# Kernel tuning notes

Hardware: AMD Instinct MI355X
Metric: run time of the kernel (lower is better)

## Reference

```python
import jax, jax.numpy as jnp
import numpy as np

EMBED_DIM = 1024
NUM_HEADS = 16
HEAD_DIM = EMBED_DIM // NUM_HEADS
SEG_LEN = 1024  # all segment_lengths equal, dilation_rate == 1


def setup_inputs() -> dict:
    key = jax.random.key(0)
    k1, k2, k3 = jax.random.split(key, 3)
    B, S, E = 2, 4096, EMBED_DIM
    x = jax.random.normal(k1, (B, S, E), dtype=jnp.float32)
    w_qkv = jax.random.normal(k2, (3 * E, E), dtype=jnp.float32) * (E ** -0.5)
    b_qkv = jnp.zeros((3 * E,), dtype=jnp.float32)
    w_out = jax.random.normal(k3, (E, E), dtype=jnp.float32) * (E ** -0.5)
    b_out = jnp.zeros((E,), dtype=jnp.float32)
    return {"x": x, "w_qkv": w_qkv, "b_qkv": b_qkv, "w_out": w_out, "b_out": b_out}


def reference(x, w_qkv, b_qkv, w_out, b_out):
    B, S, E = x.shape
    H, Dh = NUM_HEADS, HEAD_DIM
    scale = 1.0 / np.sqrt(Dh).astype(np.float32)
    # QKV projection
    qkv = x @ w_qkv.T + b_qkv                      # [B, S, 3E]
    qkv = qkv.reshape(B, S, 3, H, Dh).transpose(2, 0, 3, 1, 4)  # [3, B, H, S, Dh]
    q, k, v = qkv[0], qkv[1], qkv[2]
    # Segments tile the sequence; each query attends only within its segment
    # (block-diagonal attention; online-softmax combine across segments is
    # trivial since the segments are disjoint in the query dimension).
    n = S // SEG_LEN
    q = q.reshape(B, H, n, SEG_LEN, Dh)
    k = k.reshape(B, H, n, SEG_LEN, Dh)
    v = v.reshape(B, H, n, SEG_LEN, Dh)
    scores = jnp.einsum("bhnqd,bhnkd->bhnqk", q, k) * scale
    attn = jax.nn.softmax(scores, axis=-1)
    out = jnp.einsum("bhnqk,bhnkd->bhnqd", attn, v)  # [B, H, n, seg, Dh]
    out = out.reshape(B, H, S, Dh).transpose(0, 2, 1, 3).reshape(B, S, E)
    return out @ w_out.T + b_out
```

## Files before the change

kernel.cpp:

```cpp
#include <hip/hip_runtime.h>

typedef __bf16 bf16x8 __attribute__((ext_vector_type(8)));
typedef float f32x4 __attribute__((ext_vector_type(4)));

#define SL2E 0.18033688011112042f

__device__ __forceinline__ unsigned short f2bf(float f) {
  union { float f; unsigned u; } v; v.f = f;
  unsigned r = v.u + 0x7fffu + ((v.u >> 16) & 1u);
  return (unsigned short)(r >> 16);
}

__device__ __forceinline__ float fast_exp2(float x) {
#if __has_builtin(__builtin_amdgcn_exp2f)
  return __builtin_amdgcn_exp2f(x);
#else
  return exp2f(x);
#endif
}

__device__ __forceinline__ unsigned pack_bf2(float lo, float hi) {
  union { float f; unsigned u; } a, b;
  a.f = lo; b.f = hi;
#if __has_builtin(__builtin_amdgcn_perm)
  return __builtin_amdgcn_perm(b.u + 0x7fffu, a.u + 0x7fffu, 0x07060302u);
#else
  return ((b.u + 0x7fffu) & 0xffff0000u) | ((a.u + 0x7fffu) >> 16);
#endif
}

__device__ __forceinline__ void gload16(const unsigned short* g, unsigned short* l) {
  __builtin_amdgcn_global_load_lds(
      (const __attribute__((address_space(1))) unsigned int*)g,
      (__attribute__((address_space(3))) unsigned int*)l, 16, 0, 0);
}

__global__ __launch_bounds__(256) void f32_to_bf16_all(
    const float* __restrict__ x, const float* __restrict__ wq, const float* __restrict__ wo,
    unsigned short* __restrict__ xb, unsigned short* __restrict__ wqb, unsigned short* __restrict__ wob) {
  int i = blockIdx.x * 256 + threadIdx.x;
  const float* src; unsigned short* dst; int off;
  if (i < 2097152) { src = x; dst = xb; off = i; }
  else if (i < 2883584) { src = wq; dst = wqb; off = i - 2097152; }
  else if (i < 3145728) { src = wo; dst = wob; off = i - 2883584; }
  else return;
  float4 v = ((const float4*)src)[off];
  ushort4 o;
  o.x = f2bf(v.x); o.y = f2bf(v.y); o.z = f2bf(v.z); o.w = f2bf(v.w);
  ((ushort4*)dst)[off] = o;
}


__global__ __launch_bounds__(256) void gemm_qkv(
    const unsigned short* __restrict__ A,
    const unsigned short* __restrict__ Bt,
    const float* __restrict__ bias,
    unsigned short* __restrict__ Qb,
    unsigned short* __restrict__ Kb,
    unsigned short* __restrict__ Vtb) {
  const int K = 1024;
  __shared__ unsigned short As[128 * 64];
  __shared__ unsigned short Bs[128 * 64];
  int tid = threadIdx.x;
  int m0 = blockIdx.x * 128, n0 = blockIdx.y * 128;
  int w = tid >> 6, lane = tid & 63, l15 = lane & 15, quad = lane >> 4;
  int wm = (w & 1) * 64, wn = (w >> 1) * 64;

  f32x4 acc[4][4] = {};

  int rs = w * 32 + (lane >> 3);
  int cs = ((lane & 7) ^ (lane >> 3)) * 8;
  const unsigned short* Ag = A + (m0 + rs) * K + cs;
  const unsigned short* Bg = Bt + (n0 + rs) * K + cs;
  unsigned short* Asl = As + w * 2048;
  unsigned short* Bsl = Bs + w * 2048;

  int t = n0 >> 10;
  int b = m0 >> 12;

  if (t != 2) {
    for (int kt = 0; kt < K; kt += 64) {
      __syncthreads();
#pragma unroll
      for (int i = 0; i < 4; ++i) {
        gload16(Ag + i * 8 * K + kt, Asl + i * 512);
        gload16(Bg + i * 8 * K + kt, Bsl + i * 512);
      }
      __syncthreads();
#pragma unroll
      for (int kk = 0; kk < 2; ++kk) {
        int swk = (((kk * 4 + quad) ^ (l15 & 7))) * 8;
        bf16x8 af[4], bfr[4];
#pragma unroll
        for (int i = 0; i < 4; ++i) af[i] = *(const bf16x8*)(As + (wm + i * 16 + l15) * 64 + swk);
#pragma unroll
        for (int j = 0; j < 4; ++j) bfr[j] = *(const bf16x8*)(Bs + (wn + j * 16 + l15) * 64 + swk);
#pragma unroll
        for (int j = 0; j < 4; ++j)
#pragma unroll
          for (int i = 0; i < 4; ++i)
            acc[j][i] = __builtin_amdgcn_mfma_f32_16x16x32_bf16(bfr[j], af[i], acc[j][i], 0, 0, 0);
      }
    }
    unsigned short* dst = (t == 0) ? Qb : Kb;
    float sc = (t == 0) ? SL2E : 1.0f;
    int h = ((n0 + wn) >> 6) & 15;
    int head_base = (b * 16 + h) * 4096 * 64;
    int s_base = (m0 & 4095) + wm;
#pragma unroll
    for (int j = 0; j < 4; ++j) {
      int d0 = j * 16 + quad * 4;
      float4 bv = *(const float4*)(bias + n0 + wn + d0);
#pragma unroll
      for (int i = 0; i < 4; ++i) {
        int s = s_base + i * 16 + l15;
        ushort4 pk;
        pk.x = f2bf((acc[j][i][0] + bv.x) * sc);
        pk.y = f2bf((acc[j][i][1] + bv.y) * sc);
        pk.z = f2bf((acc[j][i][2] + bv.z) * sc);
        pk.w = f2bf((acc[j][i][3] + bv.w) * sc);
        *(ushort4*)(dst + head_base + s * 64 + d0) = pk;
      }
    }
  } else {
    for (int kt = 0; kt < K; kt += 64) {
      __syncthreads();
#pragma unroll
      for (int i = 0; i < 4; ++i) {
        gload16(Ag + i * 8 * K + kt, Asl + i * 512);
        gload16(Bg + i * 8 * K + kt, Bsl + i * 512);
      }
      __syncthreads();
#pragma unroll
      for (int kk = 0; kk < 2; ++kk) {
        int swk = (((kk * 4 + quad) ^ (l15 & 7))) * 8;
        bf16x8 af[4], bfr[4];
#pragma unroll
        for (int i = 0; i < 4; ++i) af[i] = *(const bf16x8*)(As + (wm + i * 16 + l15) * 64 + swk);
#pragma unroll
        for (int j = 0; j < 4; ++j) bfr[j] = *(const bf16x8*)(Bs + (wn + j * 16 + l15) * 64 + swk);
#pragma unroll
        for (int i = 0; i < 4; ++i)
#pragma unroll
          for (int j = 0; j < 4; ++j)
            acc[i][j] = __builtin_amdgcn_mfma_f32_16x16x32_bf16(af[i], bfr[j], acc[i][j], 0, 0, 0);
      }
    }
    int sblk = (m0 & 4095) + wm + quad * 4;
#pragma unroll
    for (int j = 0; j < 4; ++j) {
      int n_j = n0 + wn + j * 16 + l15;
      float bv = bias[n_j];
      int h = (n_j >> 6) & 15, d = n_j & 63;
      int vbase = ((b * 16 + h) * 64 + d) * 4096;
#pragma unroll
      for (int i = 0; i < 4; ++i) {
        int s = sblk + i * 16;
        ushort4 pk;
        pk.x = f2bf(acc[i][j][0] + bv);
        pk.y = f2bf(acc[i][j][1] + bv);
        pk.z = f2bf(acc[i][j][2] + bv);
        pk.w = f2bf(acc[i][j][3] + bv);
        *(ushort4*)(Vtb + vbase + s) = pk;
      }
    }
  }
}

#define LDP 72
#define SWZ(r, cg) ((((r) * 8) + ((cg) ^ ((r) & 7))) * 8)

__global__ __launch_bounds__(256) void attn_k(
    const unsigned short* __restrict__ Qb,
    const unsigned short* __restrict__ Kb,
    const unsigned short* __restrict__ Vtb,
    unsigned short* __restrict__ Ab) {
  __shared__ unsigned short KV[2][2][4096];
  __shared__ unsigned short Ps[2][4][16 * LDP];

  int tid = threadIdx.x;
  int idx = blockIdx.x;
  int grp = idx & 127, qblk = idx >> 7;
  int seg = grp & 3, h = (grp >> 2) & 15, b = grp >> 6;
  int w = tid >> 6, lane = tid & 63, l15 = lane & 15, quad = lane >> 4;
  int bh = b * 16 + h;
  int q0 = seg * 1024 + qblk * 256 + w * 64;

  const unsigned short* Kg = Kb + (bh * 4096 + seg * 1024) * 64;
  const unsigned short* Vg = Vtb + bh * 64 * 4096 + seg * 1024;

  int r0 = w * 16 + (lane >> 3);
  int cs = ((lane & 7) ^ (lane >> 3)) * 8;

  const unsigned short* Qg = Qb + (bh * 4096 + q0) * 64;
  bf16x8 qf[4][2];
#pragma unroll
  for (int qb = 0; qb < 4; ++qb)
#pragma unroll
    for (int kk = 0; kk < 2; ++kk)
      qf[qb][kk] = *(const bf16x8*)(Qg + (qb * 16 + l15) * 64 + kk * 32 + quad * 8);

  f32x4 o[4][4] = {};
  float lsum[4] = {0.f, 0.f, 0.f, 0.f};
  unsigned short* Pw0 = Ps[0][w];
  unsigned short* Pw1 = Ps[1][w];

  {
    unsigned short* dk = &KV[0][0][w * 1024];
    unsigned short* dv = &KV[0][1][w * 1024];
    gload16(Kg + r0 * 64 + cs, dk);
    gload16(Kg + (r0 + 8) * 64 + cs, dk + 512);
    gload16(Vg + r0 * 4096 + cs, dv);
    gload16(Vg + (r0 + 8) * 4096 + cs, dv + 512);
  }

#pragma unroll 2
  for (int kt = 0; kt < 16; ++kt) {
    int cur = kt & 1;
    __syncthreads();
    if (kt < 15) {
      unsigned short* dk = &KV[cur ^ 1][0][w * 1024];
      unsigned short* dv = &KV[cur ^ 1][1][w * 1024];
      const unsigned short* kN = Kg + (kt + 1) * 4096;
      const unsigned short* vN = Vg + (kt + 1) * 64;
      gload16(kN + r0 * 64 + cs, dk);
      gload16(kN + (r0 + 8) * 64 + cs, dk + 512);
      gload16(vN + r0 * 4096 + cs, dv);
      gload16(vN + (r0 + 8) * 4096 + cs, dv + 512);
    }
    const unsigned short* Kt = KV[cur][0];
    const unsigned short* Vt = KV[cur][1];

    uint2 pp[4][4];
#pragma unroll
    for (int half = 0; half < 2; ++half) {
      f32x4 st[2][4] = {};
      bf16x8 kf[2][2];
#pragma unroll
      for (int kk = 0; kk < 2; ++kk) {
        int cg = kk * 4 + quad;
        kf[kk][0] = *(const bf16x8*)(Kt + SWZ(half * 32 + l15, cg));
        kf[kk][1] = *(const bf16x8*)(Kt + SWZ(half * 32 + 16 + l15, cg));
      }
      __builtin_amdgcn_s_setprio(1);
#pragma unroll
      for (int kk = 0; kk < 2; ++kk)
#pragma unroll
        for (int qb = 0; qb < 4; ++qb) {
          st[0][qb] = __builtin_amdgcn_mfma_f32_16x16x32_bf16(kf[kk][0], qf[qb][kk], st[0][qb], 0, 0, 0);
          st[1][qb] = __builtin_amdgcn_mfma_f32_16x16x32_bf16(kf[kk][1], qf[qb][kk], st[1][qb], 0, 0, 0);
        }
      __builtin_amdgcn_s_setprio(0);
#pragma unroll
      for (int kb = 0; kb < 2; ++kb)
#pragma unroll
        for (int qb = 0; qb < 4; ++qb) {
          f32x4 s = st[kb][qb];
          float p0 = fast_exp2(s[0]), p1 = fast_exp2(s[1]);
          float p2 = fast_exp2(s[2]), p3 = fast_exp2(s[3]);
          lsum[qb] += (p0 + p1) + (p2 + p3);
          uint2 d;
          d.x = pack_bf2(p0, p1);
          d.y = pack_bf2(p2, p3);
          pp[qb][half * 2 + kb] = d;
        }
    }

#pragma unroll
    for (int g = 0; g < 4; ++g) {
      *(uint2*)(Pw0 + l15 * LDP + g * 16 + quad * 4) = pp[0][g];
      *(uint2*)(Pw1 + l15 * LDP + g * 16 + quad * 4) = pp[1][g];
    }

    bf16x8 vf[2][4];
#pragma unroll
    for (int kk = 0; kk < 2; ++kk)
#pragma unroll
      for (int db = 0; db < 4; ++db)
        vf[kk][db] = *(const bf16x8*)(Vt + SWZ(db * 16 + l15, kk * 4 + quad));

#pragma unroll
    for (int qb = 0; qb < 4; ++qb) {
      unsigned short* Pw = (qb & 1) ? Pw1 : Pw0;
      bf16x8 pa0 = *(const bf16x8*)(Pw + l15 * LDP + quad * 8);
      bf16x8 pa1 = *(const bf16x8*)(Pw + l15 * LDP + 32 + quad * 8);
      if (qb < 2) {
#pragma unroll
        for (int g = 0; g < 4; ++g)
          *(uint2*)(Pw + l15 * LDP + g * 16 + quad * 4) = pp[qb + 2][g];
      }
      __builtin_amdgcn_s_setprio(1);
#pragma unroll
      for (int db = 0; db < 4; ++db)
        o[qb][db] = __builtin_amdgcn_mfma_f32_16x16x32_bf16(pa0, vf[0][db], o[qb][db], 0, 0, 0);
#pragma unroll
      for (int db = 0; db < 4; ++db)
        o[qb][db] = __builtin_amdgcn_mfma_f32_16x16x32_bf16(pa1, vf[1][db], o[qb][db], 0, 0, 0);
      __builtin_amdgcn_s_setprio(0);
    }
  }

#pragma unroll
  for (int qb = 0; qb < 4; ++qb) {
    lsum[qb] += __shfl_xor(lsum[qb], 16);
    lsum[qb] += __shfl_xor(lsum[qb], 32);
  }

  float* Wf = (float*)(&KV[0][0][0]) + w * 1024;
#pragma unroll
  for (int qb = 0; qb < 4; ++qb) {
#pragma unroll
    for (int db = 0; db < 4; ++db)
#pragma unroll
      for (int r = 0; r < 4; ++r)
        Wf[(quad * 4 + r) * 64 + db * 16 + l15] = o[qb][db][r];
    float inv = 1.0f / lsum[qb];
    float4 x0 = *(float4*)(Wf + l15 * 64 + quad * 8);
    float4 x1 = *(float4*)(Wf + l15 * 64 + quad * 8 + 4);
    float4 x2 = *(float4*)(Wf + l15 * 64 + (quad + 4) * 8);
    float4 x3 = *(float4*)(Wf + l15 * 64 + (quad + 4) * 8 + 4);
    uint4 u0, u1;
    u0.x = pack_bf2(x0.x * inv, x0.y * inv);
    u0.y = pack_bf2(x0.z * inv, x0.w * inv);
    u0.z = pack_bf2(x1.x * inv, x1.y * inv);
    u0.w = pack_bf2(x1.z * inv, x1.w * inv);
    u1.x = pack_bf2(x2.x * inv, x2.y * inv);
    u1.y = pack_bf2(x2.z * inv, x2.w * inv);
    u1.z = pack_bf2(x3.x * inv, x3.y * inv);
    u1.w = pack_bf2(x3.z * inv, x3.w * inv);
    int sg = q0 + qb * 16 + l15;
    int base = (b * 4096 + sg) * 1024 + h * 64;
    *(uint4*)(Ab + base + quad * 8) = u0;
    *(uint4*)(Ab + base + (quad + 4) * 8) = u1;
  }
}

__global__ __launch_bounds__(256) void gemm_out(
    const unsigned short* __restrict__ A,
    const unsigned short* __restrict__ Bt,
    const float* __restrict__ bias,
    float* __restrict__ C) {
  const int K = 1024;
  __shared__ unsigned short As[128 * 64];
  __shared__ unsigned short Bs[128 * 64];
  int tid = threadIdx.x;
  int m0 = blockIdx.x * 128, n0 = blockIdx.y * 128;
  int w = tid >> 6, lane = tid & 63, l15 = lane & 15, quad = lane >> 4;
  int wm = (w & 1) * 64, wn = (w >> 1) * 64;

  f32x4 acc[4][4] = {};

  int rs = w * 32 + (lane >> 3);
  int cs = ((lane & 7) ^ (lane >> 3)) * 8;
  const unsigned short* Ag = A + (m0 + rs) * K + cs;
  const unsigned short* Bg = Bt + (n0 + rs) * K + cs;
  unsigned short* Asl = As + w * 2048;
  unsigned short* Bsl = Bs + w * 2048;

  for (int kt = 0; kt < K; kt += 64) {
    __syncthreads();
#pragma unroll
    for (int i = 0; i < 4; ++i) {
      gload16(Ag + i * 8 * K + kt, Asl + i * 512);
      gload16(Bg + i * 8 * K + kt, Bsl + i * 512);
    }
    __syncthreads();
#pragma unroll
    for (int kk = 0; kk < 2; ++kk) {
      int swk = (((kk * 4 + quad) ^ (l15 & 7))) * 8;
      bf16x8 af[4], bfr[4];
#pragma unroll
      for (int i = 0; i < 4; ++i) af[i] = *(const bf16x8*)(As + (wm + i * 16 + l15) * 64 + swk);
#pragma unroll
      for (int j = 0; j < 4; ++j) bfr[j] = *(const bf16x8*)(Bs + (wn + j * 16 + l15) * 64 + swk);
#pragma unroll
      for (int j = 0; j < 4; ++j)
#pragma unroll
        for (int i = 0; i < 4; ++i)
          acc[j][i] = __builtin_amdgcn_mfma_f32_16x16x32_bf16(bfr[j], af[i], acc[j][i], 0, 0, 0);
    }
  }

#pragma unroll
  for (int j = 0; j < 4; ++j) {
    int nb = n0 + wn + j * 16 + quad * 4;
    float4 bv = *(const float4*)(bias + nb);
#pragma unroll
    for (int i = 0; i < 4; ++i) {
      int m = m0 + wm + i * 16 + l15;
      float4 ov;
      ov.x = acc[j][i][0] + bv.x;
      ov.y = acc[j][i][1] + bv.y;
      ov.z = acc[j][i][2] + bv.z;
      ov.w = acc[j][i][3] + bv.w;
      *(float4*)(C + m * 1024 + nb) = ov;
    }
  }
}

extern "C" void kernel_launch(void* const* d_in, const int* in_sizes, int n_in,
                              void* d_out, int out_size, void* d_ws, size_t ws_size,
                              hipStream_t stream) {
  const float* x     = (const float*)d_in[0];
  const float* w_qkv = (const float*)d_in[1];
  const float* b_qkv = (const float*)d_in[2];
  const float* w_out = (const float*)d_in[3];
  const float* b_out = (const float*)d_in[4];
  float* out = (float*)d_out;
  char* ws = (char*)d_ws;

  unsigned short* wqkvb = (unsigned short*)(ws);
  unsigned short* woutb = (unsigned short*)(ws + 6291456);
  unsigned short* Qb    = (unsigned short*)(ws + 8388608);
  unsigned short* Kb    = (unsigned short*)(ws + 25165824);
  unsigned short* Vtb   = (unsigned short*)(ws + 41943040);
  unsigned short* xb    = (unsigned short*)(ws + 58720256);
  unsigned short* Ab    = xb;

  f32_to_bf16_all<<<12288, 256, 0, stream>>>(x, w_qkv, w_out, xb, wqkvb, woutb);
  gemm_qkv<<<dim3(64, 24), 256, 0, stream>>>(xb, wqkvb, b_qkv, Qb, Kb, Vtb);
  attn_k<<<512, 256, 0, stream>>>(Qb, Kb, Vtb, Ab);
  gemm_out<<<dim3(64, 8), 256, 0, stream>>>(Ab, woutb, b_out, out);
}
```

Before: 254.1 us.

## Remap attention block indices and simplify P staging to single LDS buffer

Changes the block-to-(group, qblk) mapping so neighbouring blocks share K/V segments, which is meant to improve L2 reuse. Removes the double-buffered P staging area and the s_setprio hints, writing and reading one P tile per query block in sequence. K fragments are now loaded per kk right before their MFMAs. This frees LDS and registers, but it serializes the P write and read and drops the priority scheduling, which could expose LDS latency. The new write to the same per-wave buffer relies on wave-local ordering.

```diff
diff --git a/kernel.cpp b/kernel.cpp
--- a/kernel.cpp
+++ b/kernel.cpp
@@ -176,11 +176,12 @@
     const unsigned short* __restrict__ Vtb,
     unsigned short* __restrict__ Ab) {
   __shared__ unsigned short KV[2][2][4096];
-  __shared__ unsigned short Ps[2][4][16 * LDP];
+  __shared__ unsigned short Ps[4][16 * LDP];
 
   int tid = threadIdx.x;
   int idx = blockIdx.x;
-  int grp = idx & 127, qblk = idx >> 7;
+  int grp = ((idx >> 5) << 3) | (idx & 7);
+  int qblk = (idx >> 3) & 3;
   int seg = grp & 3, h = (grp >> 2) & 15, b = grp >> 6;
   int w = tid >> 6, lane = tid & 63, l15 = lane & 15, quad = lane >> 4;
   int bh = b * 16 + h;
@@ -202,8 +203,7 @@
 
   f32x4 o[4][4] = {};
   float lsum[4] = {0.f, 0.f, 0.f, 0.f};
-  unsigned short* Pw0 = Ps[0][w];
-  unsigned short* Pw1 = Ps[1][w];
+  unsigned short* Pw = Ps[w];
 
   {
     unsigned short* dk = &KV[0][0][w * 1024];
@@ -235,22 +235,17 @@
 #pragma unroll
     for (int half = 0; half < 2; ++half) {
       f32x4 st[2][4] = {};
-      bf16x8 kf[2][2];
 #pragma unroll
       for (int kk = 0; kk < 2; ++kk) {
         int cg = kk * 4 + quad;
-        kf[kk][0] = *(const bf16x8*)(Kt + SWZ(half * 32 + l15, cg));
-        kf[kk][1] = *(const bf16x8*)(Kt + SWZ(half * 32 + 16 + l15, cg));
-      }
-      __builtin_amdgcn_s_setprio(1);
-#pragma unroll
-      for (int kk = 0; kk < 2; ++kk)
+        bf16x8 kf0 = *(const bf16x8*)(Kt + SWZ(half * 32 + l15, cg));
+        bf16x8 kf1 = *(const bf16x8*)(Kt + SWZ(half * 32 + 16 + l15, cg));
 #pragma unroll
         for (int qb = 0; qb < 4; ++qb) {
-          st[0][qb] = __builtin_amdgcn_mfma_f32_16x16x32_bf16(kf[kk][0], qf[qb][kk], st[0][qb], 0, 0, 0);
-          st[1][qb] = __builtin_amdgcn_mfma_f32_16x16x32_bf16(kf[kk][1], qf[qb][kk], st[1][qb], 0, 0, 0);
+          st[0][qb] = __builtin_amdgcn_mfma_f32_16x16x32_bf16(kf0, qf[qb][kk], st[0][qb], 0, 0, 0);
+          st[1][qb] = __builtin_amdgcn_mfma_f32_16x16x32_bf16(kf1, qf[qb][kk], st[1][qb], 0, 0, 0);
         }
-      __builtin_amdgcn_s_setprio(0);
+      }
 #pragma unroll
       for (int kb = 0; kb < 2; ++kb)
 #pragma unroll
@@ -266,37 +261,24 @@
         }
     }
 
-#pragma unroll
-    for (int g = 0; g < 4; ++g) {
-      *(uint2*)(Pw0 + l15 * LDP + g * 16 + quad * 4) = pp[0][g];
-      *(uint2*)(Pw1 + l15 * LDP + g * 16 + quad * 4) = pp[1][g];
-    }
-
     bf16x8 vf[2][4];
 #pragma unroll
     for (int kk = 0; kk < 2; ++kk)
 #pragma unroll
       for (int db = 0; db < 4; ++db)
         vf[kk][db] = *(const bf16x8*)(Vt + SWZ(db * 16 + l15, kk * 4 + quad));
-
 #pragma unroll
     for (int qb = 0; qb < 4; ++qb) {
-      unsigned short* Pw = (qb & 1) ? Pw1 : Pw0;
-      bf16x8 pa0 = *(const bf16x8*)(Pw + l15 * LDP + quad * 8);
-      bf16x8 pa1 = *(const bf16x8*)(Pw + l15 * LDP + 32 + quad * 8);
-      if (qb < 2) {
-#pragma unroll
-        for (int g = 0; g < 4; ++g)
-          *(uint2*)(Pw + l15 * LDP + g * 16 + quad * 4) = pp[qb + 2][g];
-      }
-      __builtin_amdgcn_s_setprio(1);
-#pragma unroll
-      for (int db = 0; db < 4; ++db)
-        o[qb][db] = __builtin_amdgcn_mfma_f32_16x16x32_bf16(pa0, vf[0][db], o[qb][db], 0, 0, 0);
-#pragma unroll
-      for (int db = 0; db < 4; ++db)
-        o[qb][db] = __builtin_amdgcn_mfma_f32_16x16x32_bf16(pa1, vf[1][db], o[qb][db], 0, 0, 0);
-      __builtin_amdgcn_s_setprio(0);
+#pragma unroll
+      for (int g = 0; g < 4; ++g)
+        *(uint2*)(Pw + l15 * LDP + g * 16 + quad * 4) = pp[qb][g];
+#pragma unroll
+      for (int kk = 0; kk < 2; ++kk) {
+        bf16x8 pa = *(const bf16x8*)(Pw + l15 * LDP + kk * 32 + quad * 8);
+#pragma unroll
+        for (int db = 0; db < 4; ++db)
+          o[qb][db] = __builtin_amdgcn_mfma_f32_16x16x32_bf16(pa, vf[kk][db], o[qb][db], 0, 0, 0);
+      }
     }
   }
 
```

Result: faster. 234.5 us (-7.7%).
